# Kernel tuning notes

Hardware: AMD Instinct MI355X
Metric: run time of the kernel (lower is better)

Reference implementation:

```python
import jax, jax.numpy as jnp
import numpy as np

N, E, C, D, A, F_, H, RNF = 20000, 200000, 14, 3, 16, 128, 128, 128
CONSTANT = 1.0
LN_EPS = 1e-5


def _pool_matrix(n_channel, dtype):
    ones = np.ones((n_channel, n_channel))
    mats = []
    for i in range(n_channel):
        ws = n_channel - i
        mats.append((np.triu(ones) - np.triu(ones, k=ws)) / ws)
    return jnp.asarray(np.stack(mats), dtype)  # [C, C, C]


def _scatter_mean(src, idx, n):
    s = jax.ops.segment_sum(src, idx, num_segments=n)
    cnt = jax.ops.segment_sum(jnp.ones((src.shape[0],), src.dtype), idx, num_segments=n)
    return s / jnp.maximum(cnt, 1.0).reshape((n,) + (1,) * (src.ndim - 1))


def setup_inputs() -> dict:
    key = jax.random.key(0)
    ks = jax.random.split(key, 24)
    h = jax.random.normal(ks[0], (N, F_), jnp.float32)
    x = jax.random.normal(ks[1], (N, C, D), jnp.float32)
    channel_attr = jax.random.normal(ks[2], (N, C, A), jnp.float32)
    cw = jax.random.uniform(ks[3], (N, C), jnp.float32)
    cw = cw * (jax.random.uniform(ks[4], (N, C)) > 0.3)  # some padded channels
    cw = cw.at[:, 0].set(jax.random.uniform(ks[5], (N,)) + 0.1)  # >=1 valid channel
    row = jax.random.randint(ks[6], (E,), 0, N, dtype=jnp.int32)
    col = jax.random.randint(ks[7], (E,), 0, N, dtype=jnp.int32)

    def lin(k, din, dout):
        return 0.02 * jax.random.normal(k, (din, dout), jnp.float32), jnp.zeros((dout,), jnp.float32)

    rad_w, rad_b = lin(ks[8], A * A, RNF)
    e_w1, e_b1 = lin(ks[9], 2 * F_ + RNF, H)
    e_w2, e_b2 = lin(ks[10], H, H)
    att_w, att_b = lin(ks[11], H, 1)
    c_w1, c_b1 = lin(ks[12], H, H)
    c_w2, c_b2 = lin(ks[13], H, C)
    n_w1, n_b1 = lin(ks[14], F_ + H, H)
    n_w2, n_b2 = lin(ks[15], H, F_)
    ln_g = jnp.ones((F_,), jnp.float32)
    ln_b = jnp.zeros((F_,), jnp.float32)
    return dict(h=h, x=x, channel_attr=channel_attr, channel_weights=cw, row=row, col=col,
                rad_w=rad_w, rad_b=rad_b, e_w1=e_w1, e_b1=e_b1, e_w2=e_w2, e_b2=e_b2,
                att_w=att_w, att_b=att_b, c_w1=c_w1, c_b1=c_b1, c_w2=c_w2, c_b2=c_b2,
                n_w1=n_w1, n_b1=n_b1, n_w2=n_w2, n_b2=n_b2, ln_g=ln_g, ln_b=ln_b)


def reference(h, x, channel_attr, channel_weights, row, col,
              rad_w, rad_b, e_w1, e_b1, e_w2, e_b2, att_w, att_b,
              c_w1, c_b1, c_w2, c_b2, n_w1, n_b1, n_w2, n_b2, ln_g, ln_b):
    silu = jax.nn.silu
    n_nodes = h.shape[0]

    # ---- coord2radial (NUM_SEG = 1) ----
    # pairwise channel distances per edge: [E, C, C]
    coord_msg = jnp.linalg.norm(x[row][:, :, None, :] - x[col][:, None, :, :], axis=-1)
    coord_msg = coord_msg * (channel_weights[row][:, :, None] * channel_weights[col][:, None, :])
    # attr^T @ msg @ attr -> [E, A, A] -> [E, A*A]
    radial = jnp.einsum('eca,ecd,edb->eab', channel_attr[row], coord_msg, channel_attr[col])
    radial = radial.reshape(radial.shape[0], -1)
    radial_norm = jnp.linalg.norm(radial, axis=-1, keepdims=True) + CONSTANT
    radial = (radial @ rad_w + rad_b) / radial_norm

    channel_mask = (channel_weights != 0).astype(x.dtype)  # [N, C]
    channel_sum = jnp.sum(channel_weights != 0, axis=-1).astype(jnp.int32)  # [N]
    pooled_col = (x[col] * channel_mask[col][:, :, None]).sum(1) / channel_sum[col].astype(x.dtype)[:, None]
    coord_diff = x[row] - pooled_col[:, None, :]  # [E, C, 3]

    # ---- edge MLP + attention gate ----
    ef = silu(jnp.concatenate([h[row], h[col], radial], axis=-1) @ e_w1 + e_b1)
    ef = silu(ef @ e_w2 + e_b2)
    ef = ef * jax.nn.sigmoid(ef @ att_w + att_b)  # att_mlp active (hidden_nf == input_nf)

    # ---- RollerPooling on coord_mlp output ----
    cm = silu(ef @ c_w1 + c_b1) @ c_w2 + c_b2  # [E, C]
    pool_mat = _pool_matrix(C, ef.dtype)[channel_sum[row] - 1]  # [E, C, C]
    pooled = jnp.einsum('eij,ej->ei', pool_mat, cm)  # [E, C]
    trans = coord_diff * pooled[:, :, None]  # [E, C, 3]

    x_new = x + _scatter_mean(trans, row, n_nodes)
    agg = _scatter_mean(ef, col, n_nodes)

    nh = silu(jnp.concatenate([h, agg], axis=-1) @ n_w1 + n_b1) @ n_w2 + n_b2
    hr = h + nh
    mu = hr.mean(-1, keepdims=True)
    var = ((hr - mu) ** 2).mean(-1, keepdims=True)
    h_new = (hr - mu) * jax.lax.rsqrt(var + LN_EPS) * ln_g + ln_b
    return h_new, x_new
```

## Files before the change

kernel.cpp:

```cpp
#include <hip/hip_runtime.h>
#include <hip/hip_bf16.h>


#define TM 64
#define TN 16
#define PAD 36

typedef __attribute__((ext_vector_type(8))) short bf16x8;
typedef __attribute__((ext_vector_type(4))) float f32x4;

__device__ __forceinline__ float siluf(float v) { return v / (1.f + __expf(-v)); }
__device__ __forceinline__ float sigmf(float v) { return 1.f / (1.f + __expf(-v)); }
__device__ __forceinline__ short f2bs(float f) {
  union { __hip_bfloat16 b; short s; } u;
  u.b = __float2bfloat16(f);
  return u.s;
}
__device__ __forceinline__ __hip_bfloat162 mk_bf162(float v0, float v1) {
  __hip_bfloat162 r;
  r.x = __float2bfloat16(v0);
  r.y = __float2bfloat16(v1);
  return r;
}

__global__ __launch_bounds__(256) void k_pack(
    const float* __restrict__ h, const float* __restrict__ x,
    const float* __restrict__ attr, const float* __restrict__ cw,
    const float* __restrict__ rad_w, const float* __restrict__ e_w1,
    const float* __restrict__ e_w2, const float* __restrict__ c_w1,
    const float* __restrict__ n_w1, const float* __restrict__ n_w2,
    const float* __restrict__ c_w2,
    __hip_bfloat16* __restrict__ wz_rad, __hip_bfloat16* __restrict__ wz_e1,
    __hip_bfloat16* __restrict__ wz_e2, __hip_bfloat16* __restrict__ wz_c1,
    __hip_bfloat16* __restrict__ wz_n1, __hip_bfloat16* __restrict__ wz_n2,
    __hip_bfloat16* __restrict__ wz_c2,
    __hip_bfloat16* __restrict__ attrS, __hip_bfloat16* __restrict__ hb,
    float* __restrict__ pooled_x, int* __restrict__ chsum, int Nn) {
  int idx = blockIdx.x * 256 + threadIdx.x;
  if (idx < 165888) {
    int i = idx;
    if (i >= 163840) {
      int base = i - 163840;
      int k = base >> 4, n = base & 15;
      wz_c2[(size_t)(k >> 5) * 512 + n * 32 + (k & 31)] =
          (n < 14) ? __float2bfloat16(c_w2[k * 14 + n]) : __float2bfloat16(0.f);
      return;
    }
    const float* W;
    __hip_bfloat16* O;
    int base;
    if (i < 32768) { W = rad_w; O = wz_rad; base = i; }
    else if (i < 81920) { W = e_w1; O = wz_e1; base = i - 32768; }
    else if (i < 98304) { W = e_w2; O = wz_e2; base = i - 81920; }
    else if (i < 114688) { W = c_w1; O = wz_c1; base = i - 98304; }
    else if (i < 147456) { W = n_w1; O = wz_n1; base = i - 114688; }
    else { W = n_w2; O = wz_n2; base = i - 147456; }
    int k = base >> 7, n = base & 127;
    O[(size_t)((k >> 5) * 128 + n) * 32 + (k & 31)] = __float2bfloat16(W[base]);
    return;
  }
  idx -= 165888;
  int na = Nn * 256, nh = Nn * 128;
  if (idx < na) {
    int n = idx >> 8, r = idx & 255, i2 = r >> 4, a = r & 15;
    float v = 0.f;
    if (i2 < 14) v = attr[(size_t)n * 224 + i2 * 16 + a] * cw[(size_t)n * 14 + i2];
    attrS[(size_t)n * 256 + a * 16 + i2] = __float2bfloat16(v);
    return;
  }
  idx -= na;
  if (idx < nh) {
    hb[idx] = __float2bfloat16(h[idx]);
    return;
  }
  idx -= nh;
  if (idx >= Nn) return;
  int n = idx;
  int cnt = 0;
  float sx = 0.f, sy = 0.f, sz = 0.f;
#pragma unroll
  for (int c = 0; c < 14; c++) {
    float w = cw[n * 14 + c];
    if (w != 0.f) {
      cnt++;
      sx += x[n * 42 + c * 3 + 0];
      sy += x[n * 42 + c * 3 + 1];
      sz += x[n * 42 + c * 3 + 2];
    }
  }
  chsum[n] = cnt;
  float inv = 1.f / (float)(cnt > 0 ? cnt : 1);
  pooled_x[n * 3 + 0] = sx * inv;
  pooled_x[n * 3 + 1] = sy * inv;
  pooled_x[n * 3 + 2] = sz * inv;
}

__global__ __launch_bounds__(256, 3) void k_mega(
    const __hip_bfloat16* __restrict__ hb, const float* __restrict__ x,
    const __hip_bfloat16* __restrict__ attrS,
    const int* __restrict__ row, const int* __restrict__ col,
    const float* __restrict__ pooled_x, const int* __restrict__ chsum,
    const __hip_bfloat16* __restrict__ wz_rad, const float* __restrict__ rad_b,
    const __hip_bfloat16* __restrict__ wz_e1, const float* __restrict__ e_b1,
    const __hip_bfloat16* __restrict__ wz_e2, const float* __restrict__ e_b2,
    const float* __restrict__ att_w, const float* __restrict__ att_b,
    const __hip_bfloat16* __restrict__ wz_c1, const float* __restrict__ c_b1,
    const __hip_bfloat16* __restrict__ wz_c2, const float* __restrict__ c_b2,
    unsigned* __restrict__ cnt_row, unsigned* __restrict__ cnt_col,
    __hip_bfloat162* __restrict__ x_acc, __hip_bfloat162* __restrict__ agg,
    int Ee) {
  __shared__ __hip_bfloat16 S[12][TM][32];
  __shared__ float s_att[TM];
  __shared__ float s_red[4][TM];
  __shared__ float s_rn[TM];
  __shared__ int s_row[TM], s_col[TM], s_cs[TM];
  float* s_cm   = (float*)&S[0][0][0];
  float* s_pool = (float*)&S[1][0][0];

  const int t = threadIdx.x;
  const int e0 = blockIdx.x * TM;
  const int ne = min(TM, Ee - e0);
  const int lane = t & 63, wave = t >> 6, quad = lane >> 4, mr = lane & 15;
  const int n0 = wave * 32;
  const f32x4 zacc = {0.f, 0.f, 0.f, 0.f};
  const bf16x8 zero8 = {0, 0, 0, 0, 0, 0, 0, 0};

  if (t < TM) {
    int ge = e0 + min(t, ne - 1);
    int r = row[ge], c = col[ge];
    s_row[t] = r;
    s_col[t] = c;
    s_cs[t] = chsum[r];
    if (t < ne) {
      atomicAdd(&cnt_row[r], 1u);
      atomicAdd(&cnt_col[c], 1u);
    }
  }

#pragma unroll 1
  for (int b = 0; b < 4; b++) {
    float xr0v[4], xr1v[4], xr2v[4], xc0v[4], xc1v[4], xc2v[4];
    bf16x8 bCv[4], aRv[4];
#pragma unroll
    for (int p = 0; p < 4; p++) {
      const int e = wave * 16 + b * 4 + p;
      const int ge = e0 + min(e, ne - 1);
      const int re = row[ge], ce = col[ge];
      const int mrc = min(mr, 13);
      const float* xp = x + (size_t)re * 42 + mrc * 3;
      xr0v[p] = xp[0]; xr1v[p] = xp[1]; xr2v[p] = xp[2];
      const float* xq = x + (size_t)ce * 42 + mrc * 3;
      xc0v[p] = xq[0]; xc1v[p] = xq[1]; xc2v[p] = xq[2];
      bCv[p] = zero8; aRv[p] = zero8;
      if (quad < 2) {
        bCv[p] = *(const bf16x8*)&attrS[(size_t)ce * 256 + mr * 16 + quad * 8];
        aRv[p] = *(const bf16x8*)&attrS[(size_t)re * 256 + mr * 16 + quad * 8];
      }
    }
#pragma unroll
    for (int p = 0; p < 4; p++) {
      const int e = wave * 16 + b * 4 + p;
      const float xr0 = xr0v[p], xr1 = xr1v[p], xr2 = xr2v[p];
      const float xc0 = xc0v[p], xc1 = xc1v[p], xc2 = xc2v[p];
      bf16x8 aX = zero8, bX = zero8;
      if (quad == 0) {
        aX[0] = f2bs(xc0); aX[1] = f2bs(xc1); aX[2] = f2bs(xc2);
        bX[0] = f2bs(xr0); bX[1] = f2bs(xr1); bX[2] = f2bs(xr2);
      }
      f32x4 G = __builtin_amdgcn_mfma_f32_16x16x32_bf16(aX, bX, zacc, 0, 0, 0);
      const float nr = xr0 * xr0 + xr1 * xr1 + xr2 * xr2;
      const float nc = xc0 * xc0 + xc1 * xc1 + xc2 * xc2;
      float dD[4];
#pragma unroll
      for (int r = 0; r < 4; r++) {
        float ncj = __shfl(nc, quad * 4 + r);
        dD[r] = sqrtf(fmaxf(ncj + nr - 2.f * G[r], 0.f));
      }
      bf16x8 aD;
#pragma unroll
      for (int jj = 0; jj < 8; jj++) {
        const int qs = (quad * 2 + (jj >> 2)) & 3;
        float dv = __shfl(dD[jj & 3], (qs << 4) | mr);
        if (quad >= 2) dv = 0.f;
        aD[jj] = f2bs(dv);
      }
      f32x4 m1 = __builtin_amdgcn_mfma_f32_16x16x32_bf16(aD, bCv[p], zacc, 0, 0, 0);
      bf16x8 bM;
#pragma unroll
      for (int jj = 0; jj < 8; jj++) {
        const int qs = (quad * 2 + (jj >> 2)) & 3;
        float mv = __shfl(m1[jj & 3], (qs << 4) | mr);
        if (quad >= 2) mv = 0.f;
        bM[jj] = f2bs(mv);
      }
      f32x4 rd = __builtin_amdgcn_mfma_f32_16x16x32_bf16(aRv[p], bM, zacc, 0, 0, 0);
      float ss = rd[0] * rd[0] + rd[1] * rd[1] + rd[2] * rd[2] + rd[3] * rd[3];
      ss += __shfl_xor(ss, 32); ss += __shfl_xor(ss, 16); ss += __shfl_xor(ss, 8);
      ss += __shfl_xor(ss, 4);  ss += __shfl_xor(ss, 2);  ss += __shfl_xor(ss, 1);
      if (lane == 0) s_rn[e] = sqrtf(ss) + 1.0f;
#pragma unroll
      for (int r = 0; r < 4; r++) {
        const int aa = quad * 4 + r;
        const int c = ((aa & 1) << 4) | mr;
        const int pcol = (((c >> 3) ^ ((e >> 1) & 3)) << 3) | (c & 7);
        S[aa >> 1][e][pcol] = __float2bfloat16(rd[r]);
      }
    }
  }
  __syncthreads();

  const int acol = ((quad ^ ((mr >> 1) & 3)) << 3);

  {
    f32x4 a0[4], a1[4];
#pragma unroll
    for (int mf = 0; mf < 4; mf++) { a0[mf] = zacc; a1[mf] = zacc; }
#pragma unroll
    for (int kb = 0; kb < 8; kb++) {
      const __hip_bfloat16* wp = wz_rad + ((size_t)(kb * 128 + n0 + mr) * 32 + quad * 8);
      bf16x8 b0 = *(const bf16x8*)wp;
      bf16x8 b1 = *(const bf16x8*)(wp + 16 * 32);
#pragma unroll
      for (int mf = 0; mf < 4; mf++) {
        bf16x8 a = *(const bf16x8*)&S[kb][mf * 16 + mr][acol];
        a0[mf] = __builtin_amdgcn_mfma_f32_16x16x32_bf16(a, b0, a0[mf], 0, 0, 0);
        a1[mf] = __builtin_amdgcn_mfma_f32_16x16x32_bf16(a, b1, a1[mf], 0, 0, 0);
      }
    }
    float rb0 = rad_b[n0 + mr], rb1 = rad_b[n0 + 16 + mr];
#pragma unroll
    for (int mf = 0; mf < 4; mf++)
#pragma unroll
      for (int r = 0; r < 4; r++) {
        int e = mf * 16 + quad * 4 + r;
        int es = (e >> 1) & 3;
        int c0 = (((mr >> 3) ^ es) << 3) | (mr & 7);
        int c1 = (((2 | (mr >> 3)) ^ es) << 3) | (mr & 7);
        float inv = 1.f / s_rn[e];
        S[8 + wave][e][c0] = __float2bfloat16((a0[mf][r] + rb0) * inv);
        S[8 + wave][e][c1] = __float2bfloat16((a1[mf][r] + rb1) * inv);
      }
  }
  __syncthreads();

  {
    const int m = t >> 2, part = t & 3;
    const int pc = ((part ^ ((m >> 1) & 3)) << 3);
    const __hip_bfloat16* hr = hb + (size_t)s_row[m] * 128 + part * 8;
    const __hip_bfloat16* hc = hb + (size_t)s_col[m] * 128 + part * 8;
#pragma unroll
    for (int kb = 0; kb < 4; kb++) {
      *(int4*)&S[kb][m][pc]     = *(const int4*)&hr[kb * 32];
      *(int4*)&S[4 + kb][m][pc] = *(const int4*)&hc[kb * 32];
    }
  }
  __syncthreads();

  f32x4 s1a0[4], s1a1[4];
#pragma unroll
  for (int mf = 0; mf < 4; mf++) { s1a0[mf] = zacc; s1a1[mf] = zacc; }
#pragma unroll
  for (int kb = 0; kb < 12; kb++) {
    const __hip_bfloat16* wp = wz_e1 + ((size_t)(kb * 128 + n0 + mr) * 32 + quad * 8);
    bf16x8 b0 = *(const bf16x8*)wp;
    bf16x8 b1 = *(const bf16x8*)(wp + 16 * 32);
#pragma unroll
    for (int mf = 0; mf < 4; mf++) {
      bf16x8 a = *(const bf16x8*)&S[kb][mf * 16 + mr][acol];
      s1a0[mf] = __builtin_amdgcn_mfma_f32_16x16x32_bf16(a, b0, s1a0[mf], 0, 0, 0);
      s1a1[mf] = __builtin_amdgcn_mfma_f32_16x16x32_bf16(a, b1, s1a1[mf], 0, 0, 0);
    }
  }
  __syncthreads();
  {
    float bias0 = e_b1[n0 + mr], bias1 = e_b1[n0 + 16 + mr];
#pragma unroll
    for (int mf = 0; mf < 4; mf++)
#pragma unroll
      for (int r = 0; r < 4; r++) {
        int e = mf * 16 + quad * 4 + r;
        int es = (e >> 1) & 3;
        int c0 = (((mr >> 3) ^ es) << 3) | (mr & 7);
        int c1 = (((2 | (mr >> 3)) ^ es) << 3) | (mr & 7);
        S[wave][e][c0] = __float2bfloat16(siluf(s1a0[mf][r] + bias0));
        S[wave][e][c1] = __float2bfloat16(siluf(s1a1[mf][r] + bias1));
      }
  }
  __syncthreads();

  const float aw0 = att_w[n0 + mr], aw1 = att_w[n0 + 16 + mr];
  {
    f32x4 a0[4], a1[4];
#pragma unroll
    for (int mf = 0; mf < 4; mf++) { a0[mf] = zacc; a1[mf] = zacc; }
#pragma unroll
    for (int kb = 0; kb < 4; kb++) {
      const __hip_bfloat16* wp = wz_e2 + ((size_t)(kb * 128 + n0 + mr) * 32 + quad * 8);
      bf16x8 b0 = *(const bf16x8*)wp;
      bf16x8 b1 = *(const bf16x8*)(wp + 16 * 32);
#pragma unroll
      for (int mf = 0; mf < 4; mf++) {
        bf16x8 a = *(const bf16x8*)&S[kb][mf * 16 + mr][acol];
        a0[mf] = __builtin_amdgcn_mfma_f32_16x16x32_bf16(a, b0, a0[mf], 0, 0, 0);
        a1[mf] = __builtin_amdgcn_mfma_f32_16x16x32_bf16(a, b1, a1[mf], 0, 0, 0);
      }
    }
    float bias0 = e_b2[n0 + mr], bias1 = e_b2[n0 + 16 + mr];
    float part[4][4];
#pragma unroll
    for (int mf = 0; mf < 4; mf++)
#pragma unroll
      for (int r = 0; r < 4; r++) {
        int e = mf * 16 + quad * 4 + r;
        int es = (e >> 1) & 3;
        int c0 = (((mr >> 3) ^ es) << 3) | (mr & 7);
        int c1 = (((2 | (mr >> 3)) ^ es) << 3) | (mr & 7);
        float v0 = siluf(a0[mf][r] + bias0);
        float v1 = siluf(a1[mf][r] + bias1);
        S[4 + wave][e][c0] = __float2bfloat16(v0);
        S[4 + wave][e][c1] = __float2bfloat16(v1);
        part[mf][r] = v0 * aw0 + v1 * aw1;
      }
#pragma unroll
    for (int msk = 1; msk < 16; msk <<= 1)
#pragma unroll
      for (int mf = 0; mf < 4; mf++)
#pragma unroll
        for (int r = 0; r < 4; r++) part[mf][r] += __shfl_xor(part[mf][r], msk);
    if (mr == 0) {
#pragma unroll
      for (int mf = 0; mf < 4; mf++)
#pragma unroll
        for (int r = 0; r < 4; r++)
          s_red[wave][mf * 16 + quad * 4 + r] = part[mf][r];
    }
  }
  __syncthreads();
  if (t < TM) {
    float s = s_red[0][t] + s_red[1][t] + s_red[2][t] + s_red[3][t];
    s_att[t] = sigmf(s + att_b[0]);
  }
  __syncthreads();

  {
    f32x4 a0[4], a1[4];
#pragma unroll
    for (int mf = 0; mf < 4; mf++) { a0[mf] = zacc; a1[mf] = zacc; }
#pragma unroll
    for (int kb = 0; kb < 4; kb++) {
      const __hip_bfloat16* wp = wz_c1 + ((size_t)(kb * 128 + n0 + mr) * 32 + quad * 8);
      bf16x8 b0 = *(const bf16x8*)wp;
      bf16x8 b1 = *(const bf16x8*)(wp + 16 * 32);
#pragma unroll
      for (int mf = 0; mf < 4; mf++) {
        bf16x8 a = *(const bf16x8*)&S[4 + kb][mf * 16 + mr][acol];
        a0[mf] = __builtin_amdgcn_mfma_f32_16x16x32_bf16(a, b0, a0[mf], 0, 0, 0);
        a1[mf] = __builtin_amdgcn_mfma_f32_16x16x32_bf16(a, b1, a1[mf], 0, 0, 0);
      }
    }
    float bias0 = c_b1[n0 + mr], bias1 = c_b1[n0 + 16 + mr];
#pragma unroll
    for (int mf = 0; mf < 4; mf++)
#pragma unroll
      for (int r = 0; r < 4; r++) {
        int e = mf * 16 + quad * 4 + r;
        int es = (e >> 1) & 3;
        int c0 = (((mr >> 3) ^ es) << 3) | (mr & 7);
        int c1 = (((2 | (mr >> 3)) ^ es) << 3) | (mr & 7);
        float av = s_att[e];
        S[8 + wave][e][c0] = __float2bfloat16(siluf(av * a0[mf][r] + bias0));
        S[8 + wave][e][c1] = __float2bfloat16(siluf(av * a1[mf][r] + bias1));
      }
  }
  __syncthreads();

  {
    f32x4 acc = zacc;
#pragma unroll
    for (int kb = 0; kb < 4; kb++) {
      bf16x8 a = *(const bf16x8*)&S[8 + kb][wave * 16 + mr][acol];
      bf16x8 b = *(const bf16x8*)(wz_c2 + ((size_t)(kb * 16 + mr) * 32 + quad * 8));
      acc = __builtin_amdgcn_mfma_f32_16x16x32_bf16(a, b, acc, 0, 0, 0);
    }
    if (mr < 14) {
      float bias = c_b2[mr];
#pragma unroll
      for (int r = 0; r < 4; r++)
        s_cm[(wave * 16 + quad * 4 + r) * 14 + mr] = acc[r] + bias;
    }
  }
  __syncthreads();

  for (int i = t; i < TM * 14; i += 256) {
    int e = i / 14, c = i % 14;
    int wsz = 15 - s_cs[e];
    int hi = min(c + wsz, 14);
    float s = 0.f;
    for (int j = c; j < hi; j++) s += s_cm[e * 14 + j];
    s_pool[e * 14 + c] = s / (float)wsz;
  }
  __syncthreads();

  for (int i = t; i < TM * 21; i += 256) {
    int e = i / 21, pr = i % 21;
    if (e < ne) {
      int r0 = pr * 2, r1 = r0 + 1;
      const float* xp = x + (size_t)s_row[e] * 42;
      const float* pc = pooled_x + (size_t)s_col[e] * 3;
      float v0 = (xp[r0] - pc[r0 % 3]) * s_pool[e * 14 + r0 / 3];
      float v1 = (xp[r1] - pc[r1 % 3]) * s_pool[e * 14 + r1 / 3];
      unsafeAtomicAdd(&x_acc[(size_t)s_row[e] * 21 + pr], mk_bf162(v0, v1));
    }
  }
  for (int i = t; i < TM * 64; i += 256) {
    int e = i >> 6, o2 = i & 63;
    if (e < ne) {
      float av = s_att[e];
      int c = (o2 & 15) * 2;
      int pc = (((c >> 3) ^ ((e >> 1) & 3)) << 3) | (c & 7);
      const __hip_bfloat16* wp2 = &S[4 + (o2 >> 4)][e][pc];
      float v0 = __bfloat162float(wp2[0]) * av;
      float v1 = __bfloat162float(wp2[1]) * av;
      unsafeAtomicAdd(&agg[(size_t)s_col[e] * 64 + o2], mk_bf162(v0, v1));
    }
  }
}

__global__ __launch_bounds__(256) void k_node(
    const float* __restrict__ h, const __hip_bfloat162* __restrict__ agg,
    const unsigned* __restrict__ cnt_col,
    const __hip_bfloat16* __restrict__ wz_n1, const float* __restrict__ n_b1,
    const __hip_bfloat16* __restrict__ wz_n2, const float* __restrict__ n_b2,
    const float* __restrict__ ln_g, const float* __restrict__ ln_b,
    const float* __restrict__ x, const __hip_bfloat162* __restrict__ x_acc,
    const unsigned* __restrict__ cnt_row,
    float* __restrict__ out_h, float* __restrict__ out_x, int Nn) {
  __shared__ __hip_bfloat16 sA[8][16][PAD];
  __shared__ __hip_bfloat16 sT[4][16][PAD];
  __shared__ float s_h[TN][128];
  __shared__ float s_o[TN][132];
  const int t = threadIdx.x;
  const int nb0 = blockIdx.x * TN;
  const int nn = min(TN, Nn - nb0);

  for (int i = t; i < TN * 21; i += 256) {
    int n = i / 21, pr = i % 21;
    if (n < nn) {
      int gn = nb0 + n;
      unsigned c = cnt_row[gn];
      float inv = 1.f / (float)(c > 0 ? c : 1);
      float2 xa = __bfloat1622float2(x_acc[(size_t)gn * 21 + pr]);
      size_t gi = (size_t)gn * 42 + pr * 2;
      out_x[gi]     = x[gi] + xa.x * inv;
      out_x[gi + 1] = x[gi + 1] + xa.y * inv;
    }
  }

  for (int i = t; i < TN * 64; i += 256) {
    int m = i >> 6, kp = (i & 63) << 1;
    int kb = kp >> 5, kk = kp & 31;
    int gn = nb0 + min(m, nn - 1);
    const float2 hv = *(const float2*)&h[(size_t)gn * 128 + kp];
    sA[kb][m][kk]     = __float2bfloat16(hv.x);
    sA[kb][m][kk + 1] = __float2bfloat16(hv.y);
    s_h[m][kp]     = hv.x;
    s_h[m][kp + 1] = hv.y;
    unsigned c = cnt_col[gn];
    float inv = 1.f / (float)(c > 0 ? c : 1);
    float2 gv = __bfloat1622float2(agg[(size_t)gn * 64 + (kp >> 1)]);
    sA[4 + kb][m][kk]     = __float2bfloat16(gv.x * inv);
    sA[4 + kb][m][kk + 1] = __float2bfloat16(gv.y * inv);
  }
  __syncthreads();
  const int lane = t & 63, wave = t >> 6, quad = lane >> 4, mr = lane & 15;
  const int n0 = wave * 32;
  f32x4 zacc = {0.f, 0.f, 0.f, 0.f};
  {
    f32x4 acc0 = zacc, acc1 = zacc;
#pragma unroll
    for (int kb = 0; kb < 8; kb++) {
      bf16x8 a = *(const bf16x8*)&sA[kb][mr][quad * 8];
      const __hip_bfloat16* wp = wz_n1 + ((size_t)(kb * 128 + n0 + mr) * 32 + quad * 8);
      bf16x8 b0 = *(const bf16x8*)wp;
      bf16x8 b1 = *(const bf16x8*)(wp + 16 * 32);
      acc0 = __builtin_amdgcn_mfma_f32_16x16x32_bf16(a, b0, acc0, 0, 0, 0);
      acc1 = __builtin_amdgcn_mfma_f32_16x16x32_bf16(a, b1, acc1, 0, 0, 0);
    }
    float bias0 = n_b1[n0 + mr], bias1 = n_b1[n0 + 16 + mr];
#pragma unroll
    for (int r = 0; r < 4; r++) {
      int m = quad * 4 + r;
      sT[wave][m][mr]      = __float2bfloat16(siluf(acc0[r] + bias0));
      sT[wave][m][16 + mr] = __float2bfloat16(siluf(acc1[r] + bias1));
    }
  }
  __syncthreads();
  {
    f32x4 acc0 = zacc, acc1 = zacc;
#pragma unroll
    for (int kb = 0; kb < 4; kb++) {
      bf16x8 a = *(const bf16x8*)&sT[kb][mr][quad * 8];
      const __hip_bfloat16* wp = wz_n2 + ((size_t)(kb * 128 + n0 + mr) * 32 + quad * 8);
      bf16x8 b0 = *(const bf16x8*)wp;
      bf16x8 b1 = *(const bf16x8*)(wp + 16 * 32);
      acc0 = __builtin_amdgcn_mfma_f32_16x16x32_bf16(a, b0, acc0, 0, 0, 0);
      acc1 = __builtin_amdgcn_mfma_f32_16x16x32_bf16(a, b1, acc1, 0, 0, 0);
    }
    float bias0 = n_b2[n0 + mr], bias1 = n_b2[n0 + 16 + mr];
#pragma unroll
    for (int r = 0; r < 4; r++) {
      int m = quad * 4 + r;
      s_o[m][n0 + mr]      = s_h[m][n0 + mr] + acc0[r] + bias0;
      s_o[m][n0 + 16 + mr] = s_h[m][n0 + 16 + mr] + acc1[r] + bias1;
    }
  }
  __syncthreads();
  {
    int n = t >> 4, p = t & 15;
    float v[8];
    float s = 0.f;
#pragma unroll
    for (int j = 0; j < 8; j++) {
      v[j] = s_o[n][p * 8 + j];
      s += v[j];
    }
    s += __shfl_xor(s, 1); s += __shfl_xor(s, 2);
    s += __shfl_xor(s, 4); s += __shfl_xor(s, 8);
    float mu = s * (1.f / 128.f);
    float var = 0.f;
#pragma unroll
    for (int j = 0; j < 8; j++) {
      float d = v[j] - mu;
      var += d * d;
    }
    var += __shfl_xor(var, 1); var += __shfl_xor(var, 2);
    var += __shfl_xor(var, 4); var += __shfl_xor(var, 8);
    float rs = rsqrtf(var * (1.f / 128.f) + 1e-5f);
    if (n < nn) {
      size_t base = (size_t)(nb0 + n) * 128 + p * 8;
#pragma unroll
      for (int j = 0; j < 8; j++)
        out_h[base + j] = (v[j] - mu) * rs * ln_g[p * 8 + j] + ln_b[p * 8 + j];
    }
  }
}

extern "C" void kernel_launch(void* const* d_in, const int* in_sizes, int n_in,
                              void* d_out, int out_size, void* d_ws, size_t ws_size,
                              hipStream_t stream) {
  const float* h     = (const float*)d_in[0];
  const float* x     = (const float*)d_in[1];
  const float* attr  = (const float*)d_in[2];
  const float* cw    = (const float*)d_in[3];
  const int*   row   = (const int*)d_in[4];
  const int*   col   = (const int*)d_in[5];
  const float* rad_w = (const float*)d_in[6];
  const float* rad_b = (const float*)d_in[7];
  const float* e_w1  = (const float*)d_in[8];
  const float* e_b1  = (const float*)d_in[9];
  const float* e_w2  = (const float*)d_in[10];
  const float* e_b2  = (const float*)d_in[11];
  const float* att_w = (const float*)d_in[12];
  const float* att_b = (const float*)d_in[13];
  const float* c_w1  = (const float*)d_in[14];
  const float* c_b1  = (const float*)d_in[15];
  const float* c_w2  = (const float*)d_in[16];
  const float* c_b2  = (const float*)d_in[17];
  const float* n_w1  = (const float*)d_in[18];
  const float* n_b1  = (const float*)d_in[19];
  const float* n_w2  = (const float*)d_in[20];
  const float* n_b2  = (const float*)d_in[21];
  const float* ln_g  = (const float*)d_in[22];
  const float* ln_b  = (const float*)d_in[23];

  const int N = in_sizes[0] / 128;
  const int E = in_sizes[4];

  char* ws = (char*)d_ws;
  size_t off = 0;
  auto alloc = [&](size_t bytes) {
    size_t o = off;
    off += (bytes + 255) & ~(size_t)255;
    return o;
  };
  size_t off_wzr  = alloc(32768 * sizeof(__hip_bfloat16));
  size_t off_wz1  = alloc(49152 * sizeof(__hip_bfloat16));
  size_t off_wz2  = alloc(16384 * sizeof(__hip_bfloat16));
  size_t off_wzc  = alloc(16384 * sizeof(__hip_bfloat16));
  size_t off_wzn1 = alloc(32768 * sizeof(__hip_bfloat16));
  size_t off_wzn2 = alloc(16384 * sizeof(__hip_bfloat16));
  size_t off_wzc2 = alloc(2048 * sizeof(__hip_bfloat16));
  size_t off_atS  = alloc((size_t)N * 256 * sizeof(__hip_bfloat16));
  size_t off_hb   = alloc((size_t)N * 128 * sizeof(__hip_bfloat16));
  size_t off_px   = alloc((size_t)N * 3 * sizeof(float));
  size_t off_cs   = alloc((size_t)N * sizeof(int));
  size_t off_cntr = alloc((size_t)N * sizeof(unsigned));
  size_t off_cntc = alloc((size_t)N * sizeof(unsigned));
  size_t off_xacc = alloc((size_t)N * 21 * sizeof(__hip_bfloat162));
  size_t off_agg  = alloc((size_t)N * 64 * sizeof(__hip_bfloat162));

  __hip_bfloat16* wz_rad = (__hip_bfloat16*)(ws + off_wzr);
  __hip_bfloat16* wz_e1  = (__hip_bfloat16*)(ws + off_wz1);
  __hip_bfloat16* wz_e2  = (__hip_bfloat16*)(ws + off_wz2);
  __hip_bfloat16* wz_c1  = (__hip_bfloat16*)(ws + off_wzc);
  __hip_bfloat16* wz_n1  = (__hip_bfloat16*)(ws + off_wzn1);
  __hip_bfloat16* wz_n2  = (__hip_bfloat16*)(ws + off_wzn2);
  __hip_bfloat16* wz_c2  = (__hip_bfloat16*)(ws + off_wzc2);
  __hip_bfloat16* attrS  = (__hip_bfloat16*)(ws + off_atS);
  __hip_bfloat16* hb     = (__hip_bfloat16*)(ws + off_hb);
  float* pooled_x   = (float*)(ws + off_px);
  int* chsum        = (int*)(ws + off_cs);
  unsigned* cnt_row = (unsigned*)(ws + off_cntr);
  unsigned* cnt_col = (unsigned*)(ws + off_cntc);
  __hip_bfloat162* x_acc = (__hip_bfloat162*)(ws + off_xacc);
  __hip_bfloat162* agg   = (__hip_bfloat162*)(ws + off_agg);

  (void)hipMemsetAsync(ws + off_cntr, 0, off - off_cntr, stream);

  const int pack_items = 165888 + N * 256 + N * 128 + N;
  k_pack<<<dim3((pack_items + 255) / 256), dim3(256), 0, stream>>>(
      h, x, attr, cw, rad_w, e_w1, e_w2, c_w1, n_w1, n_w2, c_w2,
      wz_rad, wz_e1, wz_e2, wz_c1, wz_n1, wz_n2, wz_c2,
      attrS, hb, pooled_x, chsum, N);
  k_mega<<<dim3((E + TM - 1) / TM), dim3(256), 0, stream>>>(
      hb, x, attrS, row, col, pooled_x, chsum,
      wz_rad, rad_b, wz_e1, e_b1, wz_e2, e_b2, att_w, att_b,
      wz_c1, c_b1, wz_c2, c_b2, cnt_row, cnt_col, x_acc, agg, E);
  k_node<<<dim3((N + TN - 1) / TN), dim3(256), 0, stream>>>(
      h, agg, cnt_col, wz_n1, n_b1, wz_n2, n_b2, ln_g, ln_b,
      x, x_acc, cnt_row, (float*)d_out, (float*)d_out + (size_t)N * 128, N);
}
```

Baseline: 388.2 us.

## Enlarge node-kernel tile to 64 rows with shared-memory reuse and bf16 h input

The node kernel now processes 64 nodes per block instead of 16. Each weight fragment loaded from global memory is reused across four MFMA row tiles, which cuts weight traffic per node. The activations come from the pre-packed bf16 h buffer, one shared array with an XOR swizzle replaces the separate padded buffers, and the residual is read from global h in the LayerNorm step. This raises register pressure (launch bounds set to 3 blocks per SM) and cuts the block count to about 313. The node kernel is a small part of the total time, since the edge kernel dominates.

Result: no change. 395.8 us (+1.9%).

```diff
diff --git a/kernel.cpp b/kernel.cpp
--- a/kernel.cpp
+++ b/kernel.cpp
@@ -3,7 +3,7 @@
 
 
 #define TM 64
-#define TN 16
+#define TN 64
 #define PAD 36
 
 typedef __attribute__((ext_vector_type(8))) short bf16x8;
@@ -426,8 +426,9 @@
   }
 }
 
-__global__ __launch_bounds__(256) void k_node(
-    const float* __restrict__ h, const __hip_bfloat162* __restrict__ agg,
+__global__ __launch_bounds__(256, 3) void k_node(
+    const float* __restrict__ h, const __hip_bfloat16* __restrict__ hb,
+    const __hip_bfloat162* __restrict__ agg,
     const unsigned* __restrict__ cnt_col,
     const __hip_bfloat16* __restrict__ wz_n1, const float* __restrict__ n_b1,
     const __hip_bfloat16* __restrict__ wz_n2, const float* __restrict__ n_b2,
@@ -435,13 +436,15 @@
     const float* __restrict__ x, const __hip_bfloat162* __restrict__ x_acc,
     const unsigned* __restrict__ cnt_row,
     float* __restrict__ out_h, float* __restrict__ out_x, int Nn) {
-  __shared__ __hip_bfloat16 sA[8][16][PAD];
-  __shared__ __hip_bfloat16 sT[4][16][PAD];
-  __shared__ float s_h[TN][128];
-  __shared__ float s_o[TN][132];
+  __shared__ __hip_bfloat16 S[12][TN][32];
+  float* s_o = (float*)&S[0][0][0];
+
   const int t = threadIdx.x;
   const int nb0 = blockIdx.x * TN;
   const int nn = min(TN, Nn - nb0);
+  const int lane = t & 63, wave = t >> 6, quad = lane >> 4, mr = lane & 15;
+  const int n0 = wave * 32;
+  const f32x4 zacc = {0.f, 0.f, 0.f, 0.f};
 
   for (int i = t; i < TN * 21; i += 256) {
     int n = i / 21, pr = i % 21;
@@ -456,91 +459,126 @@
     }
   }
 
-  for (int i = t; i < TN * 64; i += 256) {
-    int m = i >> 6, kp = (i & 63) << 1;
-    int kb = kp >> 5, kk = kp & 31;
-    int gn = nb0 + min(m, nn - 1);
-    const float2 hv = *(const float2*)&h[(size_t)gn * 128 + kp];
-    sA[kb][m][kk]     = __float2bfloat16(hv.x);
-    sA[kb][m][kk + 1] = __float2bfloat16(hv.y);
-    s_h[m][kp]     = hv.x;
-    s_h[m][kp + 1] = hv.y;
+  {
+    const int m = t >> 2, part = t & 3;
+    const int gn = nb0 + min(m, nn - 1);
+    const int pc = ((part ^ ((m >> 1) & 3)) << 3);
+    const __hip_bfloat16* hr = hb + (size_t)gn * 128 + part * 8;
     unsigned c = cnt_col[gn];
     float inv = 1.f / (float)(c > 0 ? c : 1);
-    float2 gv = __bfloat1622float2(agg[(size_t)gn * 64 + (kp >> 1)]);
-    sA[4 + kb][m][kk]     = __float2bfloat16(gv.x * inv);
-    sA[4 + kb][m][kk + 1] = __float2bfloat16(gv.y * inv);
-  }
-  __syncthreads();
-  const int lane = t & 63, wave = t >> 6, quad = lane >> 4, mr = lane & 15;
-  const int n0 = wave * 32;
-  f32x4 zacc = {0.f, 0.f, 0.f, 0.f};
-  {
-    f32x4 acc0 = zacc, acc1 = zacc;
+    const __hip_bfloat162* ag = agg + (size_t)gn * 64 + part * 4;
+#pragma unroll
+    for (int kb = 0; kb < 4; kb++) {
+      *(int4*)&S[kb][m][pc] = *(const int4*)&hr[kb * 32];
+      __hip_bfloat162 g0 = ag[kb * 16 + 0];
+      __hip_bfloat162 g1 = ag[kb * 16 + 1];
+      __hip_bfloat162 g2 = ag[kb * 16 + 2];
+      __hip_bfloat162 g3 = ag[kb * 16 + 3];
+      __hip_bfloat16* dst = &S[4 + kb][m][pc];
+      float2 f0 = __bfloat1622float2(g0);
+      float2 f1 = __bfloat1622float2(g1);
+      float2 f2 = __bfloat1622float2(g2);
+      float2 f3 = __bfloat1622float2(g3);
+      dst[0] = __float2bfloat16(f0.x * inv);
+      dst[1] = __float2bfloat16(f0.y * inv);
+      dst[2] = __float2bfloat16(f1.x * inv);
+      dst[3] = __float2bfloat16(f1.y * inv);
+      dst[4] = __float2bfloat16(f2.x * inv);
+      dst[5] = __float2bfloat16(f2.y * inv);
+      dst[6] = __float2bfloat16(f3.x * inv);
+      dst[7] = __float2bfloat16(f3.y * inv);
+    }
+  }
+  __syncthreads();
+
+  const int acol = ((quad ^ ((mr >> 1) & 3)) << 3);
+
+  {
+    f32x4 a0[4], a1[4];
+#pragma unroll
+    for (int mf = 0; mf < 4; mf++) { a0[mf] = zacc; a1[mf] = zacc; }
 #pragma unroll
     for (int kb = 0; kb < 8; kb++) {
-      bf16x8 a = *(const bf16x8*)&sA[kb][mr][quad * 8];
       const __hip_bfloat16* wp = wz_n1 + ((size_t)(kb * 128 + n0 + mr) * 32 + quad * 8);
       bf16x8 b0 = *(const bf16x8*)wp;
       bf16x8 b1 = *(const bf16x8*)(wp + 16 * 32);
-      acc0 = __builtin_amdgcn_mfma_f32_16x16x32_bf16(a, b0, acc0, 0, 0, 0);
-      acc1 = __builtin_amdgcn_mfma_f32_16x16x32_bf16(a, b1, acc1, 0, 0, 0);
+#pragma unroll
+      for (int mf = 0; mf < 4; mf++) {
+        bf16x8 a = *(const bf16x8*)&S[kb][mf * 16 + mr][acol];
+        a0[mf] = __builtin_amdgcn_mfma_f32_16x16x32_bf16(a, b0, a0[mf], 0, 0, 0);
+        a1[mf] = __builtin_amdgcn_mfma_f32_16x16x32_bf16(a, b1, a1[mf], 0, 0, 0);
+      }
     }
     float bias0 = n_b1[n0 + mr], bias1 = n_b1[n0 + 16 + mr];
 #pragma unroll
-    for (int r = 0; r < 4; r++) {
-      int m = quad * 4 + r;
-      sT[wave][m][mr]      = __float2bfloat16(siluf(acc0[r] + bias0));
-      sT[wave][m][16 + mr] = __float2bfloat16(siluf(acc1[r] + bias1));
-    }
-  }
-  __syncthreads();
-  {
-    f32x4 acc0 = zacc, acc1 = zacc;
+    for (int mf = 0; mf < 4; mf++)
+#pragma unroll
+      for (int r = 0; r < 4; r++) {
+        int e = mf * 16 + quad * 4 + r;
+        int es = (e >> 1) & 3;
+        int c0 = (((mr >> 3) ^ es) << 3) | (mr & 7);
+        int c1 = (((2 | (mr >> 3)) ^ es) << 3) | (mr & 7);
+        S[8 + wave][e][c0] = __float2bfloat16(siluf(a0[mf][r] + bias0));
+        S[8 + wave][e][c1] = __float2bfloat16(siluf(a1[mf][r] + bias1));
+      }
+  }
+  __syncthreads();
+
+  {
+    f32x4 a0[4], a1[4];
+#pragma unroll
+    for (int mf = 0; mf < 4; mf++) { a0[mf] = zacc; a1[mf] = zacc; }
 #pragma unroll
     for (int kb = 0; kb < 4; kb++) {
-      bf16x8 a = *(const bf16x8*)&sT[kb][mr][quad * 8];
       const __hip_bfloat16* wp = wz_n2 + ((size_t)(kb * 128 + n0 + mr) * 32 + quad * 8);
       bf16x8 b0 = *(const bf16x8*)wp;
       bf16x8 b1 = *(const bf16x8*)(wp + 16 * 32);
-      acc0 = __builtin_amdgcn_mfma_f32_16x16x32_bf16(a, b0, acc0, 0, 0, 0);
-      acc1 = __builtin_amdgcn_mfma_f32_16x16x32_bf16(a, b1, acc1, 0, 0, 0);
+#pragma unroll
+      for (int mf = 0; mf < 4; mf++) {
+        bf16x8 a = *(const bf16x8*)&S[8 + kb][mf * 16 + mr][acol];
+        a0[mf] = __builtin_amdgcn_mfma_f32_16x16x32_bf16(a, b0, a0[mf], 0, 0, 0);
+        a1[mf] = __builtin_amdgcn_mfma_f32_16x16x32_bf16(a, b1, a1[mf], 0, 0, 0);
+      }
     }
     float bias0 = n_b2[n0 + mr], bias1 = n_b2[n0 + 16 + mr];
 #pragma unroll
-    for (int r = 0; r < 4; r++) {
-      int m = quad * 4 + r;
-      s_o[m][n0 + mr]      = s_h[m][n0 + mr] + acc0[r] + bias0;
-      s_o[m][n0 + 16 + mr] = s_h[m][n0 + 16 + mr] + acc1[r] + bias1;
-    }
-  }
-  __syncthreads();
-  {
-    int n = t >> 4, p = t & 15;
-    float v[8];
+    for (int mf = 0; mf < 4; mf++)
+#pragma unroll
+      for (int r = 0; r < 4; r++) {
+        int e = mf * 16 + quad * 4 + r;
+        s_o[e * 128 + n0 + mr]      = a0[mf][r] + bias0;
+        s_o[e * 128 + n0 + 16 + mr] = a1[mf][r] + bias1;
+      }
+  }
+  __syncthreads();
+
+  {
+    int n = t >> 2, q = t & 3;
+    int gn = nb0 + min(n, nn - 1);
+    const float* hp = h + (size_t)gn * 128 + q * 32;
+    const float* op = s_o + n * 128 + q * 32;
+    float v[32];
     float s = 0.f;
 #pragma unroll
-    for (int j = 0; j < 8; j++) {
-      v[j] = s_o[n][p * 8 + j];
+    for (int j = 0; j < 32; j++) {
+      v[j] = hp[j] + op[j];
       s += v[j];
     }
     s += __shfl_xor(s, 1); s += __shfl_xor(s, 2);
-    s += __shfl_xor(s, 4); s += __shfl_xor(s, 8);
     float mu = s * (1.f / 128.f);
     float var = 0.f;
 #pragma unroll
-    for (int j = 0; j < 8; j++) {
+    for (int j = 0; j < 32; j++) {
       float d = v[j] - mu;
       var += d * d;
     }
     var += __shfl_xor(var, 1); var += __shfl_xor(var, 2);
-    var += __shfl_xor(var, 4); var += __shfl_xor(var, 8);
     float rs = rsqrtf(var * (1.f / 128.f) + 1e-5f);
     if (n < nn) {
-      size_t base = (size_t)(nb0 + n) * 128 + p * 8;
-#pragma unroll
-      for (int j = 0; j < 8; j++)
-        out_h[base + j] = (v[j] - mu) * rs * ln_g[p * 8 + j] + ln_b[p * 8 + j];
+      size_t base = (size_t)gn * 128 + q * 32;
+#pragma unroll
+      for (int j = 0; j < 32; j++)
+        out_h[base + j] = (v[j] - mu) * rs * ln_g[q * 32 + j] + ln_b[q * 32 + j];
     }
   }
 }
@@ -627,6 +665,6 @@
       wz_rad, rad_b, wz_e1, e_b1, wz_e2, e_b2, att_w, att_b,
       wz_c1, c_b1, wz_c2, c_b2, cnt_row, cnt_col, x_acc, agg, E);
   k_node<<<dim3((N + TN - 1) / TN), dim3(256), 0, stream>>>(
-      h, agg, cnt_col, wz_n1, n_b1, wz_n2, n_b2, ln_g, ln_b,
+      h, hb, agg, cnt_col, wz_n1, n_b1, wz_n2, n_b2, ln_g, ln_b,
       x, x_acc, cnt_row, (float*)d_out, (float*)d_out + (size_t)N * 128, N);
 }
```

## Interleave weight columns for paired bf16 stores and use 16x16x16 MFMA for radial

Applied to the files above, without the earlier changes.

Weight packing now permutes output columns within each 32-column group so that each lane's two MFMA output columns are adjacent. Epilogues can then write both as one bf16x2 store and load biases as float2. The radial/Gram stage swaps the 16x16x32 MFMA and its cross-lane shuffle repacking for the 16x16x16 bf16_1k variant with 4-element operands, which removes many shuffles and the padding-zero handling. The column permutation has to stay consistent with every consumer of the packed weights and biases, including the node kernel's output indexing.

Result: faster. 349.9 us (-9.9%).

```diff
diff --git a/kernel.cpp b/kernel.cpp
--- a/kernel.cpp
+++ b/kernel.cpp
@@ -7,6 +7,7 @@
 #define PAD 36
 
 typedef __attribute__((ext_vector_type(8))) short bf16x8;
+typedef __attribute__((ext_vector_type(4))) short bf16x4;
 typedef __attribute__((ext_vector_type(4))) float f32x4;
 
 __device__ __forceinline__ float siluf(float v) { return v / (1.f + __expf(-v)); }
@@ -56,7 +57,8 @@
     else if (i < 147456) { W = n_w1; O = wz_n1; base = i - 114688; }
     else { W = n_w2; O = wz_n2; base = i - 147456; }
     int k = base >> 7, n = base & 127;
-    O[(size_t)((k >> 5) * 128 + n) * 32 + (k & 31)] = __float2bfloat16(W[base]);
+    int nr_ = ((n >> 5) << 5) | ((n & 1) << 4) | ((n & 31) >> 1);
+    O[(size_t)((k >> 5) * 128 + nr_) * 32 + (k & 31)] = __float2bfloat16(W[base]);
     return;
   }
   idx -= 165888;
@@ -123,7 +125,7 @@
   const int lane = t & 63, wave = t >> 6, quad = lane >> 4, mr = lane & 15;
   const int n0 = wave * 32;
   const f32x4 zacc = {0.f, 0.f, 0.f, 0.f};
-  const bf16x8 zero8 = {0, 0, 0, 0, 0, 0, 0, 0};
+  const bf16x4 zero4 = {0, 0, 0, 0};
 
   if (t < TM) {
     int ge = e0 + min(t, ne - 1);
@@ -140,7 +142,7 @@
 #pragma unroll 1
   for (int b = 0; b < 4; b++) {
     float xr0v[4], xr1v[4], xr2v[4], xc0v[4], xc1v[4], xc2v[4];
-    bf16x8 bCv[4], aRv[4];
+    bf16x4 bCv[4], aRv[4];
 #pragma unroll
     for (int p = 0; p < 4; p++) {
       const int e = wave * 16 + b * 4 + p;
@@ -151,49 +153,33 @@
       xr0v[p] = xp[0]; xr1v[p] = xp[1]; xr2v[p] = xp[2];
       const float* xq = x + (size_t)ce * 42 + mrc * 3;
       xc0v[p] = xq[0]; xc1v[p] = xq[1]; xc2v[p] = xq[2];
-      bCv[p] = zero8; aRv[p] = zero8;
-      if (quad < 2) {
-        bCv[p] = *(const bf16x8*)&attrS[(size_t)ce * 256 + mr * 16 + quad * 8];
-        aRv[p] = *(const bf16x8*)&attrS[(size_t)re * 256 + mr * 16 + quad * 8];
-      }
+      bCv[p] = *(const bf16x4*)&attrS[(size_t)ce * 256 + mr * 16 + quad * 4];
+      aRv[p] = *(const bf16x4*)&attrS[(size_t)re * 256 + mr * 16 + quad * 4];
     }
 #pragma unroll
     for (int p = 0; p < 4; p++) {
       const int e = wave * 16 + b * 4 + p;
       const float xr0 = xr0v[p], xr1 = xr1v[p], xr2 = xr2v[p];
       const float xc0 = xc0v[p], xc1 = xc1v[p], xc2 = xc2v[p];
-      bf16x8 aX = zero8, bX = zero8;
+      const float nr = xr0 * xr0 + xr1 * xr1 + xr2 * xr2;
+      const float nc = xc0 * xc0 + xc1 * xc1 + xc2 * xc2;
+      bf16x4 aX = zero4, bX = zero4;
       if (quad == 0) {
         aX[0] = f2bs(xc0); aX[1] = f2bs(xc1); aX[2] = f2bs(xc2);
         bX[0] = f2bs(xr0); bX[1] = f2bs(xr1); bX[2] = f2bs(xr2);
       }
-      f32x4 G = __builtin_amdgcn_mfma_f32_16x16x32_bf16(aX, bX, zacc, 0, 0, 0);
-      const float nr = xr0 * xr0 + xr1 * xr1 + xr2 * xr2;
-      const float nc = xc0 * xc0 + xc1 * xc1 + xc2 * xc2;
-      float dD[4];
+      f32x4 G = __builtin_amdgcn_mfma_f32_16x16x16bf16_1k(aX, bX, zacc, 0, 0, 0);
+      bf16x4 aM;
 #pragma unroll
       for (int r = 0; r < 4; r++) {
         float ncj = __shfl(nc, quad * 4 + r);
-        dD[r] = sqrtf(fmaxf(ncj + nr - 2.f * G[r], 0.f));
-      }
-      bf16x8 aD;
-#pragma unroll
-      for (int jj = 0; jj < 8; jj++) {
-        const int qs = (quad * 2 + (jj >> 2)) & 3;
-        float dv = __shfl(dD[jj & 3], (qs << 4) | mr);
-        if (quad >= 2) dv = 0.f;
-        aD[jj] = f2bs(dv);
-      }
-      f32x4 m1 = __builtin_amdgcn_mfma_f32_16x16x32_bf16(aD, bCv[p], zacc, 0, 0, 0);
-      bf16x8 bM;
-#pragma unroll
-      for (int jj = 0; jj < 8; jj++) {
-        const int qs = (quad * 2 + (jj >> 2)) & 3;
-        float mv = __shfl(m1[jj & 3], (qs << 4) | mr);
-        if (quad >= 2) mv = 0.f;
-        bM[jj] = f2bs(mv);
-      }
-      f32x4 rd = __builtin_amdgcn_mfma_f32_16x16x32_bf16(aRv[p], bM, zacc, 0, 0, 0);
+        aM[r] = f2bs(sqrtf(fmaxf(ncj + nr - 2.f * G[r], 0.f)));
+      }
+      f32x4 m1 = __builtin_amdgcn_mfma_f32_16x16x16bf16_1k(aM, bCv[p], zacc, 0, 0, 0);
+      bf16x4 bM;
+#pragma unroll
+      for (int r = 0; r < 4; r++) bM[r] = f2bs(m1[r]);
+      f32x4 rd = __builtin_amdgcn_mfma_f32_16x16x16bf16_1k(aRv[p], bM, zacc, 0, 0, 0);
       float ss = rd[0] * rd[0] + rd[1] * rd[1] + rd[2] * rd[2] + rd[3] * rd[3];
       ss += __shfl_xor(ss, 32); ss += __shfl_xor(ss, 16); ss += __shfl_xor(ss, 8);
       ss += __shfl_xor(ss, 4);  ss += __shfl_xor(ss, 2);  ss += __shfl_xor(ss, 1);
@@ -210,6 +196,7 @@
   __syncthreads();
 
   const int acol = ((quad ^ ((mr >> 1) & 3)) << 3);
+  const int m2 = 2 * mr;
 
   {
     f32x4 a0[4], a1[4];
@@ -227,18 +214,16 @@
         a1[mf] = __builtin_amdgcn_mfma_f32_16x16x32_bf16(a, b1, a1[mf], 0, 0, 0);
       }
     }
-    float rb0 = rad_b[n0 + mr], rb1 = rad_b[n0 + 16 + mr];
+    const float2 rbp = *(const float2*)&rad_b[n0 + m2];
 #pragma unroll
     for (int mf = 0; mf < 4; mf++)
 #pragma unroll
       for (int r = 0; r < 4; r++) {
         int e = mf * 16 + quad * 4 + r;
-        int es = (e >> 1) & 3;
-        int c0 = (((mr >> 3) ^ es) << 3) | (mr & 7);
-        int c1 = (((2 | (mr >> 3)) ^ es) << 3) | (mr & 7);
+        int pc2 = ((((m2) >> 3) ^ ((e >> 1) & 3)) << 3) | (m2 & 7);
         float inv = 1.f / s_rn[e];
-        S[8 + wave][e][c0] = __float2bfloat16((a0[mf][r] + rb0) * inv);
-        S[8 + wave][e][c1] = __float2bfloat16((a1[mf][r] + rb1) * inv);
+        *(__hip_bfloat162*)&S[8 + wave][e][pc2] =
+            mk_bf162((a0[mf][r] + rbp.x) * inv, (a1[mf][r] + rbp.y) * inv);
       }
   }
   __syncthreads();
@@ -273,22 +258,20 @@
   }
   __syncthreads();
   {
-    float bias0 = e_b1[n0 + mr], bias1 = e_b1[n0 + 16 + mr];
+    const float2 b1p = *(const float2*)&e_b1[n0 + m2];
 #pragma unroll
     for (int mf = 0; mf < 4; mf++)
 #pragma unroll
       for (int r = 0; r < 4; r++) {
         int e = mf * 16 + quad * 4 + r;
-        int es = (e >> 1) & 3;
-        int c0 = (((mr >> 3) ^ es) << 3) | (mr & 7);
-        int c1 = (((2 | (mr >> 3)) ^ es) << 3) | (mr & 7);
-        S[wave][e][c0] = __float2bfloat16(siluf(s1a0[mf][r] + bias0));
-        S[wave][e][c1] = __float2bfloat16(siluf(s1a1[mf][r] + bias1));
-      }
-  }
-  __syncthreads();
-
-  const float aw0 = att_w[n0 + mr], aw1 = att_w[n0 + 16 + mr];
+        int pc2 = (((m2 >> 3) ^ ((e >> 1) & 3)) << 3) | (m2 & 7);
+        *(__hip_bfloat162*)&S[wave][e][pc2] =
+            mk_bf162(siluf(s1a0[mf][r] + b1p.x), siluf(s1a1[mf][r] + b1p.y));
+      }
+  }
+  __syncthreads();
+
+  const float2 awp = *(const float2*)&att_w[n0 + m2];
   {
     f32x4 a0[4], a1[4];
 #pragma unroll
@@ -305,21 +288,18 @@
         a1[mf] = __builtin_amdgcn_mfma_f32_16x16x32_bf16(a, b1, a1[mf], 0, 0, 0);
       }
     }
-    float bias0 = e_b2[n0 + mr], bias1 = e_b2[n0 + 16 + mr];
+    const float2 b2p = *(const float2*)&e_b2[n0 + m2];
     float part[4][4];
 #pragma unroll
     for (int mf = 0; mf < 4; mf++)
 #pragma unroll
       for (int r = 0; r < 4; r++) {
         int e = mf * 16 + quad * 4 + r;
-        int es = (e >> 1) & 3;
-        int c0 = (((mr >> 3) ^ es) << 3) | (mr & 7);
-        int c1 = (((2 | (mr >> 3)) ^ es) << 3) | (mr & 7);
-        float v0 = siluf(a0[mf][r] + bias0);
-        float v1 = siluf(a1[mf][r] + bias1);
-        S[4 + wave][e][c0] = __float2bfloat16(v0);
-        S[4 + wave][e][c1] = __float2bfloat16(v1);
-        part[mf][r] = v0 * aw0 + v1 * aw1;
+        int pc2 = (((m2 >> 3) ^ ((e >> 1) & 3)) << 3) | (m2 & 7);
+        float v0 = siluf(a0[mf][r] + b2p.x);
+        float v1 = siluf(a1[mf][r] + b2p.y);
+        *(__hip_bfloat162*)&S[4 + wave][e][pc2] = mk_bf162(v0, v1);
+        part[mf][r] = v0 * awp.x + v1 * awp.y;
       }
 #pragma unroll
     for (int msk = 1; msk < 16; msk <<= 1)
@@ -358,18 +338,16 @@
         a1[mf] = __builtin_amdgcn_mfma_f32_16x16x32_bf16(a, b1, a1[mf], 0, 0, 0);
       }
     }
-    float bias0 = c_b1[n0 + mr], bias1 = c_b1[n0 + 16 + mr];
+    const float2 cbp = *(const float2*)&c_b1[n0 + m2];
 #pragma unroll
     for (int mf = 0; mf < 4; mf++)
 #pragma unroll
       for (int r = 0; r < 4; r++) {
         int e = mf * 16 + quad * 4 + r;
-        int es = (e >> 1) & 3;
-        int c0 = (((mr >> 3) ^ es) << 3) | (mr & 7);
-        int c1 = (((2 | (mr >> 3)) ^ es) << 3) | (mr & 7);
+        int pc2 = (((m2 >> 3) ^ ((e >> 1) & 3)) << 3) | (m2 & 7);
         float av = s_att[e];
-        S[8 + wave][e][c0] = __float2bfloat16(siluf(av * a0[mf][r] + bias0));
-        S[8 + wave][e][c1] = __float2bfloat16(siluf(av * a1[mf][r] + bias1));
+        *(__hip_bfloat162*)&S[8 + wave][e][pc2] =
+            mk_bf162(siluf(av * a0[mf][r] + cbp.x), siluf(av * a1[mf][r] + cbp.y));
       }
   }
   __syncthreads();
@@ -474,6 +452,7 @@
   __syncthreads();
   const int lane = t & 63, wave = t >> 6, quad = lane >> 4, mr = lane & 15;
   const int n0 = wave * 32;
+  const int m2 = 2 * mr;
   f32x4 zacc = {0.f, 0.f, 0.f, 0.f};
   {
     f32x4 acc0 = zacc, acc1 = zacc;
@@ -486,12 +465,12 @@
       acc0 = __builtin_amdgcn_mfma_f32_16x16x32_bf16(a, b0, acc0, 0, 0, 0);
       acc1 = __builtin_amdgcn_mfma_f32_16x16x32_bf16(a, b1, acc1, 0, 0, 0);
     }
-    float bias0 = n_b1[n0 + mr], bias1 = n_b1[n0 + 16 + mr];
+    const float2 b1p = *(const float2*)&n_b1[n0 + m2];
 #pragma unroll
     for (int r = 0; r < 4; r++) {
       int m = quad * 4 + r;
-      sT[wave][m][mr]      = __float2bfloat16(siluf(acc0[r] + bias0));
-      sT[wave][m][16 + mr] = __float2bfloat16(siluf(acc1[r] + bias1));
+      *(__hip_bfloat162*)&sT[wave][m][m2] =
+          mk_bf162(siluf(acc0[r] + b1p.x), siluf(acc1[r] + b1p.y));
     }
   }
   __syncthreads();
@@ -506,12 +485,12 @@
       acc0 = __builtin_amdgcn_mfma_f32_16x16x32_bf16(a, b0, acc0, 0, 0, 0);
       acc1 = __builtin_amdgcn_mfma_f32_16x16x32_bf16(a, b1, acc1, 0, 0, 0);
     }
-    float bias0 = n_b2[n0 + mr], bias1 = n_b2[n0 + 16 + mr];
+    const float2 b2p = *(const float2*)&n_b2[n0 + m2];
 #pragma unroll
     for (int r = 0; r < 4; r++) {
       int m = quad * 4 + r;
-      s_o[m][n0 + mr]      = s_h[m][n0 + mr] + acc0[r] + bias0;
-      s_o[m][n0 + 16 + mr] = s_h[m][n0 + 16 + mr] + acc1[r] + bias1;
+      s_o[m][n0 + m2]     = s_h[m][n0 + m2] + acc0[r] + b2p.x;
+      s_o[m][n0 + m2 + 1] = s_h[m][n0 + m2 + 1] + acc1[r] + b2p.y;
     }
   }
   __syncthreads();
```
